# Optimization experiments

Hardware: AMD Instinct MI355X
Metric: run time of the kernel (lower is better)

The kernel has to match this reference:

```python
import jax, jax.numpy as jnp
import numpy as np

B_J0 = 0.01
BETA = 1.8
GAMMA = 0.5
LENS = 0.5
HIGHT = 0.15
SCALE = 6.0
H1, H2, D_IN, D_OUT = 256, 256, 700, 20
BATCH, T = 128, 250


def spike_fn(x):
    # forward of ActFun_adp: Heaviside
    return (x > 0).astype(x.dtype)


def mem_update_adp(inputs, mem, spike, tau_adp, b, tau_m):
    alpha = jnp.exp(-1.0 / tau_m)
    ro = jnp.exp(-1.0 / tau_adp)
    b = ro * b + (1.0 - ro) * spike
    B = B_J0 + BETA * b
    mem = mem * alpha + (1.0 - alpha) * inputs - B * spike
    spike = spike_fn(mem - B)
    return mem, spike, b


def setup_inputs() -> dict:
    key = jax.random.key(0)
    ks = jax.random.split(key, 16)
    inp = {
        "x": jax.random.uniform(ks[0], (BATCH, T, D_IN), jnp.float32),
        "mem1_0": jax.random.uniform(ks[1], (BATCH, H1), jnp.float32),
        "mem2_0": jax.random.uniform(ks[2], (BATCH, H2), jnp.float32),
        "memo_0": jax.random.uniform(ks[3], (BATCH, D_OUT), jnp.float32),
        "Wi1": jax.random.normal(ks[4], (H1, D_IN), jnp.float32) * 0.05,
        "bi1": jnp.zeros((H1,), jnp.float32),
        "W11": jax.random.normal(ks[5], (H1, H1), jnp.float32) * 0.05,
        "b11": jnp.zeros((H1,), jnp.float32),
        "W12": jax.random.normal(ks[6], (H2, H1), jnp.float32) * 0.05,
        "b12": jnp.zeros((H2,), jnp.float32),
        "W22": jax.random.normal(ks[7], (H2, H2), jnp.float32) * 0.05,
        "b22": jnp.zeros((H2,), jnp.float32),
        "Wo": jax.random.normal(ks[8], (D_OUT, H2), jnp.float32) * 0.05,
        "bo": jnp.zeros((D_OUT,), jnp.float32),
        "tau_adp_h1": 150.0 + 10.0 * jax.random.normal(ks[9], (H1,), jnp.float32),
        "tau_adp_h2": 150.0 + 10.0 * jax.random.normal(ks[10], (H2,), jnp.float32),
        "tau_m_h1": 20.0 + 5.0 * jax.random.normal(ks[11], (H1,), jnp.float32),
        "tau_m_h2": 20.0 + 5.0 * jax.random.normal(ks[12], (H2,), jnp.float32),
        "tau_m_o": 20.0 + 5.0 * jax.random.normal(ks[13], (D_OUT,), jnp.float32),
    }
    return inp


def reference(x, mem1_0, mem2_0, memo_0, Wi1, bi1, W11, b11, W12, b12,
              W22, b22, Wo, bo, tau_adp_h1, tau_adp_h2, tau_m_h1, tau_m_h2, tau_m_o):
    B = x.shape[0]
    sp1_0 = jnp.zeros_like(mem1_0)
    sp2_0 = jnp.zeros_like(mem2_0)
    b1_0 = jnp.full_like(mem1_0, B_J0)
    b2_0 = jnp.full_like(mem2_0, B_J0)
    acc0 = jnp.zeros((B, Wo.shape[0]), x.dtype)
    alpha_o = jnp.exp(-1.0 / tau_m_o)

    def step(carry, inp):
        x_t, i = inp
        mem1, sp1, b1, mem2, sp2, b2, memo, acc = carry
        h1_in = x_t @ Wi1.T + bi1 + sp1 @ W11.T + b11
        mem1, sp1, b1 = mem_update_adp(h1_in, mem1, sp1, tau_adp_h1, b1, tau_m_h1)
        h2_in = sp1 @ W12.T + b12 + sp2 @ W22.T + b22
        mem2, sp2, b2 = mem_update_adp(h2_in, mem2, sp2, tau_adp_h2, b2, tau_m_h2)
        memo = memo * alpha_o + (1.0 - alpha_o) * (sp2 @ Wo.T + bo)
        acc = acc + jnp.where(i > 10, jax.nn.softmax(memo, axis=1), 0.0)
        return (mem1, sp1, b1, mem2, sp2, b2, memo, acc), None

    xs = jnp.swapaxes(x, 0, 1)  # [T, B, D_in]
    ts = jnp.arange(xs.shape[0])
    carry, _ = jax.lax.scan(step, (mem1_0, sp1_0, b1_0, mem2_0, sp2_0, b2_0, memo_0, acc0), (xs, ts))
    return carry[-1]  # accumulated softmax output [B, D_out]
```

## Files before the change

### kernel.cpp

```cpp
#include <hip/hip_runtime.h>
#include <math.h>

#define BATCH 128
#define T 250
#define D_IN 700
#define H 256
#define D_OUT 20

typedef float v2f __attribute__((ext_vector_type(2)));
typedef __attribute__((ext_vector_type(8))) short bf16x8;
typedef __attribute__((ext_vector_type(4))) float f32x4;
typedef __attribute__((ext_vector_type(4))) unsigned u32x4;

static __device__ __forceinline__ unsigned short f2b(float f) {
    unsigned u = __float_as_uint(f);
    u += 0x7FFFu + ((u >> 16) & 1u);
    return (unsigned short)(u >> 16);
}

static __device__ __forceinline__ void bar() {
    asm volatile("s_waitcnt lgkmcnt(0)" ::: "memory");
    __builtin_amdgcn_s_barrier();
    asm volatile("" ::: "memory");
}

#define PIDX(c) (10 * ((c) >> 3) + ((c) & 7))

#define N_C  (257 * 512)
#define N_WP (256 * 704)

__global__ void prep_k(const float* __restrict__ Wi1, const float* __restrict__ W11,
                       const float* __restrict__ W12, const float* __restrict__ W22,
                       const float* __restrict__ Wo,
                       unsigned short* __restrict__ Wi1p, unsigned short* __restrict__ C1,
                       unsigned short* __restrict__ C2) {
    int idx = blockIdx.x * 256 + threadIdx.x;
    if (idx < N_C) {
        int k = idx >> 9, p = idx & 511;
        float v = 0.f;
        if (k < H) v = (p < 256) ? W12[p * H + k] : W11[(p - 256) * H + k];
        C1[idx] = f2b(v);
        return;
    }
    idx -= N_C;
    if (idx < N_C) {
        int k = idx >> 9, p = idx & 511;
        float v = 0.f;
        if (k < H) {
            if (p < 256) v = W22[p * H + k];
            else if (p - 256 < D_OUT) v = Wo[(p - 256) * H + k];
        }
        C2[idx] = f2b(v);
        return;
    }
    idx -= N_C;
    if (idx < N_WP) {
        int h = idx / 704, k = idx - h * 704;
        Wi1p[idx] = (k < D_IN) ? f2b(Wi1[h * D_IN + k]) : (unsigned short)0;
    }
}

__global__ __launch_bounds__(256) void gemm_u_k(const float* __restrict__ x,
                                                const unsigned short* __restrict__ Wi1p,
                                                const float* __restrict__ bi1,
                                                float* __restrict__ U) {
    const int lane = threadIdx.x & 63;
    const int wv = threadIdx.x >> 6;
    const int quad = lane >> 4;
    const int nl = lane & 15;
    const int mbase = blockIdx.x * 64 + wv * 16;
    const int m = mbase + nl;

    f32x4 acc[16];
#pragma unroll
    for (int i = 0; i < 16; ++i) acc[i] = (f32x4)(0.f);

    float bias[16];
#pragma unroll
    for (int nt = 0; nt < 16; ++nt) bias[nt] = bi1[nt * 16 + nl];

    const float* xrow = x + (size_t)m * D_IN;
    const unsigned short* brow = Wi1p + nl * 704 + quad * 8;

    for (int k0 = 0; k0 < 704; k0 += 32) {
        int ka = k0 + quad * 8;
        int ka2 = (ka + 4 <= 696) ? ka + 4 : 696;
        float4 q0 = *(const float4*)(xrow + ka);
        float4 q1 = *(const float4*)(xrow + ka2);
        bf16x8 af;
        af[0] = (short)f2b(q0.x); af[1] = (short)f2b(q0.y);
        af[2] = (short)f2b(q0.z); af[3] = (short)f2b(q0.w);
        af[4] = (short)f2b(q1.x); af[5] = (short)f2b(q1.y);
        af[6] = (short)f2b(q1.z); af[7] = (short)f2b(q1.w);

        const unsigned short* bp = brow + k0;
        bf16x8 bf[16];
#pragma unroll
        for (int nt = 0; nt < 16; ++nt)
            bf[nt] = *(const bf16x8*)(bp + nt * 16 * 704);
#pragma unroll
        for (int nt = 0; nt < 16; ++nt)
            acc[nt] = __builtin_amdgcn_mfma_f32_16x16x32_bf16(af, bf[nt], acc[nt], 0, 0, 0);
    }

#pragma unroll
    for (int nt = 0; nt < 16; ++nt) {
#pragma unroll
        for (int r = 0; r < 4; ++r) {
            U[(size_t)(mbase + quad * 4 + r) * H + nt * 16 + nl] = acc[nt][r] + bias[nt];
        }
    }
}

static __device__ __forceinline__ void ld8b(const unsigned* __restrict__ L, int c,
                                            const unsigned short* __restrict__ Cb,
                                            unsigned l8, u32x4* b) {
    uint4 ia = *(const uint4*)(L + c);
    uint4 ib = *(const uint4*)(L + c + 4);
    unsigned I[8] = {ia.x, ia.y, ia.z, ia.w, ib.x, ib.y, ib.z, ib.w};
#pragma unroll
    for (int jj = 0; jj < 8; ++jj)
        b[jj] = *(const u32x4*)(Cb + ((unsigned)I[jj] << 9) + l8);
}

static __device__ __forceinline__ void acc8b(const u32x4* b, v2f* a) {
#pragma unroll
    for (int jj = 0; jj < 8; ++jj) {
#pragma unroll
        for (int q = 0; q < 4; ++q) {
            unsigned u = b[jj][q];
            v2f t;
            t.x = __uint_as_float(u << 16);
            t.y = __uint_as_float(u & 0xffff0000u);
            a[q] += t;
        }
    }
}

static __device__ __forceinline__ void gatherB(const unsigned* __restrict__ L, int n,
                                               const unsigned short* __restrict__ Cb,
                                               unsigned l8, v2f* a) {
    a[0] = (v2f)(0.f); a[1] = (v2f)(0.f); a[2] = (v2f)(0.f); a[3] = (v2f)(0.f);
    int nr = (n + 7) & ~7;
    if (nr == 0) return;
    u32x4 x[8], y[8];
    ld8b(L, 0, Cb, l8, x);
    if (nr == 8) { acc8b(x, a); return; }
    ld8b(L, 8, Cb, l8, y);
    int c = 16;
    for (; c + 16 <= nr; c += 16) {
        acc8b(x, a); ld8b(L, c, Cb, l8, x);
        acc8b(y, a); ld8b(L, c + 8, Cb, l8, y);
    }
    if (nr - c == 8) {
        acc8b(x, a); ld8b(L, c, Cb, l8, x);
        acc8b(y, a); acc8b(x, a);
    } else {
        acc8b(x, a); acc8b(y, a);
    }
}

__global__ __launch_bounds__(512, 1) void recurrent_k(
    const float* __restrict__ U,
    const float* __restrict__ mem1_0, const float* __restrict__ mem2_0,
    const float* __restrict__ memo_0,
    const float* __restrict__ b11v, const float* __restrict__ b12v,
    const float* __restrict__ b22v, const float* __restrict__ bov,
    const float* __restrict__ tau_adp_h1, const float* __restrict__ tau_adp_h2,
    const float* __restrict__ tau_m_h1, const float* __restrict__ tau_m_h2,
    const float* __restrict__ tau_m_o,
    const unsigned short* __restrict__ C1b, const unsigned short* __restrict__ C2b,
    float* __restrict__ out)
{
    const int tid = threadIdx.x;
    const int lane = tid & 63;
    const int w = tid >> 6;
    const bool trackA = (w < 4);
    const int wt = w & 3;
    const int bi = blockIdx.x;
    const int j = wt * 64 + lane;
    const unsigned l8 = (unsigned)lane * 8;

    __shared__ float PA[4][2][640];
    __shared__ float PB[4][3][640];
    __shared__ __align__(16) unsigned lists[8][128];

    for (int i = tid; i < 4 * 2 * 640; i += 512) ((float*)PA)[i] = 0.f;
    for (int i = tid; i < 4 * 3 * 640; i += 512) ((float*)PB)[i] = 0.f;
    __syncthreads();

    float mem1 = 0.f, b1 = 0.01f, spk1 = 0.f;
    float al1 = 0.f, ro1 = 0.f, oma1 = 0.f, omr1 = 0.f, b11p = 0.f;
    if (trackA) {
        mem1 = mem1_0[bi * H + j];
        al1 = __expf(-1.f / tau_m_h1[j]);
        ro1 = __expf(-1.f / tau_adp_h1[j]);
        oma1 = 1.f - al1; omr1 = 1.f - ro1;
        b11p = b11v[j];
    }

    float mem2 = 0.f, b2 = 0.01f, spk2 = 0.f;
    float al2 = 0.f, ro2 = 0.f, oma2 = 0.f, omr2 = 0.f, bs2 = 0.f;
    if (!trackA) {
        mem2 = mem2_0[bi * H + j];
        al2 = __expf(-1.f / tau_m_h2[j]);
        ro2 = __expf(-1.f / tau_adp_h2[j]);
        oma2 = 1.f - al2; omr2 = 1.f - ro2;
        bs2 = b12v[j] + b22v[j];
    }

    float memo = 0.f, alo = 0.f, omo = 0.f, bop = 0.f, acco = 0.f;
    const bool outl = (w == 4 && lane < D_OUT);
    if (outl) {
        memo = memo_0[bi * D_OUT + lane];
        alo = __expf(-1.f / tau_m_o[lane]);
        omo = 1.f - alo;
        bop = bov[lane];
    }

    const float* Up = U + (size_t)bi * T * H + j;
    float u_cur = trackA ? *Up : 0.f;
    float u_nxt = 0.f;
    const unsigned long long below = (1ull << lane) - 1ull;

    const int pidx_self = 320 + PIDX(j);
    const int pidx_j = PIDX(j);
    const int pidx_out = 320 + PIDX(lane);

    for (int t = 0; t < 252; ++t) {
        const int rbA = (t + 1) & 1;
        const int wbA = t & 1;
        const int rsB = (t + 1) % 3;
        const int wsB = (t + 2) % 3;

        if (trackA && t < 250) {
            float g11 = PA[0][rbA][pidx_self] + PA[1][rbA][pidx_self] +
                        PA[2][rbA][pidx_self] + PA[3][rbA][pidx_self];
            float h1 = u_cur + b11p + g11;
            b1 = ro1 * b1 + omr1 * spk1;
            float B1 = 0.01f + 1.8f * b1;
            mem1 = mem1 * al1 + oma1 * h1 - B1 * spk1;
            spk1 = (mem1 - B1 > 0.f) ? 1.f : 0.f;

            unsigned long long m = __ballot(spk1 != 0.f);
            int n = __popcll(m);
            unsigned* L = lists[w];
            if (spk1 != 0.f) L[__popcll(m & below)] = (unsigned)j;
            L[n + lane] = 256u;
            asm volatile("s_waitcnt lgkmcnt(0)" ::: "memory");
            __builtin_amdgcn_wave_barrier();

            u_nxt = Up[H];
            Up += H;

            v2f a[4];
            gatherB(L, n, C1b, l8, a);

            float* pw = &PA[wt][wbA][10 * lane];
            *(v2f*)(pw + 0) = a[0];
            *(v2f*)(pw + 2) = a[1];
            *(v2f*)(pw + 4) = a[2];
            *(v2f*)(pw + 6) = a[3];
            u_cur = u_nxt;
        }

        if (w == 4 && t >= 2) {
            float e = 0.f;
            if (lane < D_OUT) {
                float aO = PB[0][rsB][pidx_out] + PB[1][rsB][pidx_out] +
                           PB[2][rsB][pidx_out] + PB[3][rsB][pidx_out];
                memo = memo * alo + omo * (bop + aO);
                e = __expf(memo);
            }
            if (t >= 13) {
                float s = e;
#pragma unroll
                for (int dd = 16; dd >= 1; dd >>= 1) s += __shfl_xor(s, dd, 32);
                if (lane < D_OUT) acco += __fdividef(e, s);
            }
        }

        if (!trackA && t >= 1 && t < 251) {
            float g12 = PA[0][rbA][pidx_j] + PA[1][rbA][pidx_j] +
                        PA[2][rbA][pidx_j] + PA[3][rbA][pidx_j];
            float g22 = PB[0][rsB][pidx_j] + PB[1][rsB][pidx_j] +
                        PB[2][rsB][pidx_j] + PB[3][rsB][pidx_j];
            float h2 = bs2 + g22 + g12;
            b2 = ro2 * b2 + omr2 * spk2;
            float B2 = 0.01f + 1.8f * b2;
            mem2 = mem2 * al2 + oma2 * h2 - B2 * spk2;
            spk2 = (mem2 - B2 > 0.f) ? 1.f : 0.f;

            unsigned long long m = __ballot(spk2 != 0.f);
            int n = __popcll(m);
            unsigned* L = lists[w];
            if (spk2 != 0.f) L[__popcll(m & below)] = (unsigned)j;
            L[n + lane] = 256u;
            asm volatile("s_waitcnt lgkmcnt(0)" ::: "memory");
            __builtin_amdgcn_wave_barrier();

            v2f a[4];
            gatherB(L, n, C2b, l8, a);

            float* pw = &PB[wt][wsB][10 * lane];
            *(v2f*)(pw + 0) = a[0];
            *(v2f*)(pw + 2) = a[1];
            *(v2f*)(pw + 4) = a[2];
            *(v2f*)(pw + 6) = a[3];
        }

        bar();
    }

    if (outl) out[bi * D_OUT + lane] = acco;
}

extern "C" void kernel_launch(void* const* d_in, const int* in_sizes, int n_in,
                              void* d_out, int out_size, void* d_ws, size_t ws_size,
                              hipStream_t stream) {
    const float* x          = (const float*)d_in[0];
    const float* mem1_0     = (const float*)d_in[1];
    const float* mem2_0     = (const float*)d_in[2];
    const float* memo_0     = (const float*)d_in[3];
    const float* Wi1        = (const float*)d_in[4];
    const float* bi1        = (const float*)d_in[5];
    const float* W11        = (const float*)d_in[6];
    const float* b11        = (const float*)d_in[7];
    const float* W12        = (const float*)d_in[8];
    const float* b12        = (const float*)d_in[9];
    const float* W22        = (const float*)d_in[10];
    const float* b22        = (const float*)d_in[11];
    const float* Wo         = (const float*)d_in[12];
    const float* bo         = (const float*)d_in[13];
    const float* tau_adp_h1 = (const float*)d_in[14];
    const float* tau_adp_h2 = (const float*)d_in[15];
    const float* tau_m_h1   = (const float*)d_in[16];
    const float* tau_m_h2   = (const float*)d_in[17];
    const float* tau_m_o    = (const float*)d_in[18];

    float* U = (float*)d_ws;
    unsigned short* C1b = (unsigned short*)(U + ((size_t)BATCH * T + 1) * H);
    unsigned short* C2b = C1b + N_C;
    unsigned short* Wi1p = C2b + N_C;

    int prep_total = 2 * N_C + N_WP;
    prep_k<<<(prep_total + 255) / 256, 256, 0, stream>>>(
        Wi1, W11, W12, W22, Wo, Wi1p, C1b, C2b);

    gemm_u_k<<<(BATCH * T) / 64, 256, 0, stream>>>(x, Wi1p, bi1, U);

    recurrent_k<<<BATCH, 512, 0, stream>>>(U, mem1_0, mem2_0, memo_0,
                                           b11, b12, b22, bo,
                                           tau_adp_h1, tau_adp_h2,
                                           tau_m_h1, tau_m_h2, tau_m_o,
                                           C1b, C2b, (float*)d_out);
}
```

Before: 384.9 us.

## Fuse input projection GEMM into recurrent kernel and shrink layer-2 gather payload

Removes the separate gemm_u_k launch and the U buffer in global memory. Instead, each recurrent block computes its own 16-timestep chunk of x·Wi1ᵀ with MFMA, interleaved across the idle parts of each step, and double-buffers the result in LDS. It also narrows the C2 table from 512 to 288 columns so the layer-2 gather loads only W22 plus the 20 output columns, shrinking the PB layout. The trade-off is extra per-step latency and more register and LDS pressure inside the serial recurrent loop, which runs only 128 blocks.

```diff
diff --git a/kernel.cpp b/kernel.cpp
--- a/kernel.cpp
+++ b/kernel.cpp
@@ -25,8 +25,10 @@
 }
 
 #define PIDX(c) (10 * ((c) >> 3) + ((c) & 7))
-
-#define N_C  (257 * 512)
+#define QIDX(c) (6 * ((c) >> 2) + ((c) & 3))
+
+#define N_C1 (257 * 512)
+#define N_C2 (257 * 288)
 #define N_WP (256 * 704)
 
 __global__ void prep_k(const float* __restrict__ Wi1, const float* __restrict__ W11,
@@ -35,16 +37,16 @@
                        unsigned short* __restrict__ Wi1p, unsigned short* __restrict__ C1,
                        unsigned short* __restrict__ C2) {
     int idx = blockIdx.x * 256 + threadIdx.x;
-    if (idx < N_C) {
+    if (idx < N_C1) {
         int k = idx >> 9, p = idx & 511;
         float v = 0.f;
         if (k < H) v = (p < 256) ? W12[p * H + k] : W11[(p - 256) * H + k];
         C1[idx] = f2b(v);
         return;
     }
-    idx -= N_C;
-    if (idx < N_C) {
-        int k = idx >> 9, p = idx & 511;
+    idx -= N_C1;
+    if (idx < N_C2) {
+        int k = idx / 288, p = idx - k * 288;
         float v = 0.f;
         if (k < H) {
             if (p < 256) v = W22[p * H + k];
@@ -53,62 +55,10 @@
         C2[idx] = f2b(v);
         return;
     }
-    idx -= N_C;
+    idx -= N_C2;
     if (idx < N_WP) {
         int h = idx / 704, k = idx - h * 704;
         Wi1p[idx] = (k < D_IN) ? f2b(Wi1[h * D_IN + k]) : (unsigned short)0;
-    }
-}
-
-__global__ __launch_bounds__(256) void gemm_u_k(const float* __restrict__ x,
-                                                const unsigned short* __restrict__ Wi1p,
-                                                const float* __restrict__ bi1,
-                                                float* __restrict__ U) {
-    const int lane = threadIdx.x & 63;
-    const int wv = threadIdx.x >> 6;
-    const int quad = lane >> 4;
-    const int nl = lane & 15;
-    const int mbase = blockIdx.x * 64 + wv * 16;
-    const int m = mbase + nl;
-
-    f32x4 acc[16];
-#pragma unroll
-    for (int i = 0; i < 16; ++i) acc[i] = (f32x4)(0.f);
-
-    float bias[16];
-#pragma unroll
-    for (int nt = 0; nt < 16; ++nt) bias[nt] = bi1[nt * 16 + nl];
-
-    const float* xrow = x + (size_t)m * D_IN;
-    const unsigned short* brow = Wi1p + nl * 704 + quad * 8;
-
-    for (int k0 = 0; k0 < 704; k0 += 32) {
-        int ka = k0 + quad * 8;
-        int ka2 = (ka + 4 <= 696) ? ka + 4 : 696;
-        float4 q0 = *(const float4*)(xrow + ka);
-        float4 q1 = *(const float4*)(xrow + ka2);
-        bf16x8 af;
-        af[0] = (short)f2b(q0.x); af[1] = (short)f2b(q0.y);
-        af[2] = (short)f2b(q0.z); af[3] = (short)f2b(q0.w);
-        af[4] = (short)f2b(q1.x); af[5] = (short)f2b(q1.y);
-        af[6] = (short)f2b(q1.z); af[7] = (short)f2b(q1.w);
-
-        const unsigned short* bp = brow + k0;
-        bf16x8 bf[16];
-#pragma unroll
-        for (int nt = 0; nt < 16; ++nt)
-            bf[nt] = *(const bf16x8*)(bp + nt * 16 * 704);
-#pragma unroll
-        for (int nt = 0; nt < 16; ++nt)
-            acc[nt] = __builtin_amdgcn_mfma_f32_16x16x32_bf16(af, bf[nt], acc[nt], 0, 0, 0);
-    }
-
-#pragma unroll
-    for (int nt = 0; nt < 16; ++nt) {
-#pragma unroll
-        for (int r = 0; r < 4; ++r) {
-            U[(size_t)(mbase + quad * 4 + r) * H + nt * 16 + nl] = acc[nt][r] + bias[nt];
-        }
     }
 }
 
@@ -160,8 +110,62 @@
     }
 }
 
+static __device__ __forceinline__ void ld8c(const unsigned* __restrict__ L, int c,
+                                            const unsigned short* __restrict__ Cb,
+                                            unsigned mo, unsigned ao,
+                                            uint2* m, unsigned* av) {
+    uint4 ia = *(const uint4*)(L + c);
+    uint4 ib = *(const uint4*)(L + c + 4);
+    unsigned I[8] = {ia.x, ia.y, ia.z, ia.w, ib.x, ib.y, ib.z, ib.w};
+#pragma unroll
+    for (int jj = 0; jj < 8; ++jj) {
+        const unsigned short* p = Cb + (unsigned)I[jj] * 288u;
+        m[jj] = *(const uint2*)(p + mo);
+        av[jj] = *(const unsigned*)(p + ao);
+    }
+}
+
+static __device__ __forceinline__ void acc8c(const uint2* m, const unsigned* av,
+                                             v2f* g, v2f& aA) {
+#pragma unroll
+    for (int jj = 0; jj < 8; ++jj) {
+        unsigned u0 = m[jj].x, u1 = m[jj].y, uA = av[jj];
+        v2f t0, t1, tA;
+        t0.x = __uint_as_float(u0 << 16); t0.y = __uint_as_float(u0 & 0xffff0000u);
+        t1.x = __uint_as_float(u1 << 16); t1.y = __uint_as_float(u1 & 0xffff0000u);
+        tA.x = __uint_as_float(uA << 16); tA.y = __uint_as_float(uA & 0xffff0000u);
+        g[0] += t0; g[1] += t1; aA += tA;
+    }
+}
+
+static __device__ __forceinline__ void gather2(const unsigned* __restrict__ L, int n,
+                                               const unsigned short* __restrict__ Cb,
+                                               unsigned mo, unsigned ao,
+                                               v2f* g, v2f& aA) {
+    g[0] = (v2f)(0.f); g[1] = (v2f)(0.f); aA = (v2f)(0.f);
+    int nr = (n + 7) & ~7;
+    if (nr == 0) return;
+    uint2 xm[8], ym[8]; unsigned xa[8], ya[8];
+    ld8c(L, 0, Cb, mo, ao, xm, xa);
+    if (nr == 8) { acc8c(xm, xa, g, aA); return; }
+    ld8c(L, 8, Cb, mo, ao, ym, ya);
+    int c = 16;
+    for (; c + 16 <= nr; c += 16) {
+        acc8c(xm, xa, g, aA); ld8c(L, c, Cb, mo, ao, xm, xa);
+        acc8c(ym, ya, g, aA); ld8c(L, c + 8, Cb, mo, ao, ym, ya);
+    }
+    if (nr - c == 8) {
+        acc8c(xm, xa, g, aA); ld8c(L, c, Cb, mo, ao, xm, xa);
+        acc8c(ym, ya, g, aA); acc8c(xm, xa, g, aA);
+    } else {
+        acc8c(xm, xa, g, aA); acc8c(ym, ya, g, aA);
+    }
+}
+
 __global__ __launch_bounds__(512, 1) void recurrent_k(
-    const float* __restrict__ U,
+    const float* __restrict__ x,
+    const unsigned short* __restrict__ Wi1p,
+    const float* __restrict__ bi1,
     const float* __restrict__ mem1_0, const float* __restrict__ mem2_0,
     const float* __restrict__ memo_0,
     const float* __restrict__ b11v, const float* __restrict__ b12v,
@@ -180,14 +184,18 @@
     const int bi = blockIdx.x;
     const int j = wt * 64 + lane;
     const unsigned l8 = (unsigned)lane * 8;
+    const unsigned mo = (unsigned)lane * 4;
+    const unsigned ao = 256u + 2u * (unsigned)(lane & 15);
+    const int quad = lane >> 4;
+    const int nl = lane & 15;
 
     __shared__ float PA[4][2][640];
-    __shared__ float PB[4][3][640];
+    __shared__ float PB[4][3][432];
+    __shared__ float Ubuf[2][16][260];
     __shared__ __align__(16) unsigned lists[8][128];
 
     for (int i = tid; i < 4 * 2 * 640; i += 512) ((float*)PA)[i] = 0.f;
-    for (int i = tid; i < 4 * 3 * 640; i += 512) ((float*)PB)[i] = 0.f;
-    __syncthreads();
+    for (int i = tid; i < 4 * 3 * 432; i += 512) ((float*)PB)[i] = 0.f;
 
     float mem1 = 0.f, b1 = 0.01f, spk1 = 0.f;
     float al1 = 0.f, ro1 = 0.f, oma1 = 0.f, omr1 = 0.f, b11p = 0.f;
@@ -218,14 +226,46 @@
         bop = bov[lane];
     }
 
-    const float* Up = U + (size_t)bi * T * H + j;
-    float u_cur = trackA ? *Up : 0.f;
-    float u_nxt = 0.f;
+    f32x4 uacc[2];
+    uacc[0] = (f32x4)(0.f); uacc[1] = (f32x4)(0.f);
+    float ubias[2];
+    ubias[0] = bi1[w * 32 + nl];
+    ubias[1] = bi1[w * 32 + 16 + nl];
+    const float* xb = x + (size_t)bi * T * D_IN;
+
+    {
+#pragma unroll 1
+        for (int kc = 0; kc < 22; ++kc) {
+            int ka = kc * 32 + quad * 8;
+            int ka2 = (ka + 4 <= 696) ? ka + 4 : 696;
+            const float* xrow = xb + (size_t)nl * D_IN;
+            float4 q0 = *(const float4*)(xrow + ka);
+            float4 q1 = *(const float4*)(xrow + ka2);
+            bf16x8 af;
+            af[0] = (short)f2b(q0.x); af[1] = (short)f2b(q0.y);
+            af[2] = (short)f2b(q0.z); af[3] = (short)f2b(q0.w);
+            af[4] = (short)f2b(q1.x); af[5] = (short)f2b(q1.y);
+            af[6] = (short)f2b(q1.z); af[7] = (short)f2b(q1.w);
+#pragma unroll
+            for (int tt = 0; tt < 2; ++tt) {
+                bf16x8 bfv = *(const bf16x8*)(Wi1p + (size_t)(w * 32 + tt * 16 + nl) * 704 + ka);
+                uacc[tt] = __builtin_amdgcn_mfma_f32_16x16x32_bf16(af, bfv, uacc[tt], 0, 0, 0);
+            }
+        }
+#pragma unroll
+        for (int tt = 0; tt < 2; ++tt)
+#pragma unroll
+            for (int r = 0; r < 4; ++r)
+                Ubuf[0][quad * 4 + r][w * 32 + tt * 16 + nl] = uacc[tt][r] + ubias[tt];
+        uacc[0] = (f32x4)(0.f); uacc[1] = (f32x4)(0.f);
+    }
+    __syncthreads();
+
     const unsigned long long below = (1ull << lane) - 1ull;
-
     const int pidx_self = 320 + PIDX(j);
     const int pidx_j = PIDX(j);
-    const int pidx_out = 320 + PIDX(lane);
+    const int qidx_j = QIDX(j);
+    const int qidx_out = 384 + 6 * (lane >> 2) + (lane & 3);
 
     for (int t = 0; t < 252; ++t) {
         const int rbA = (t + 1) & 1;
@@ -236,7 +276,8 @@
         if (trackA && t < 250) {
             float g11 = PA[0][rbA][pidx_self] + PA[1][rbA][pidx_self] +
                         PA[2][rbA][pidx_self] + PA[3][rbA][pidx_self];
-            float h1 = u_cur + b11p + g11;
+            float u = Ubuf[(t >> 4) & 1][t & 15][j];
+            float h1 = u + b11p + g11;
             b1 = ro1 * b1 + omr1 * spk1;
             float B1 = 0.01f + 1.8f * b1;
             mem1 = mem1 * al1 + oma1 * h1 - B1 * spk1;
@@ -250,9 +291,6 @@
             asm volatile("s_waitcnt lgkmcnt(0)" ::: "memory");
             __builtin_amdgcn_wave_barrier();
 
-            u_nxt = Up[H];
-            Up += H;
-
             v2f a[4];
             gatherB(L, n, C1b, l8, a);
 
@@ -261,14 +299,13 @@
             *(v2f*)(pw + 2) = a[1];
             *(v2f*)(pw + 4) = a[2];
             *(v2f*)(pw + 6) = a[3];
-            u_cur = u_nxt;
         }
 
         if (w == 4 && t >= 2) {
             float e = 0.f;
             if (lane < D_OUT) {
-                float aO = PB[0][rsB][pidx_out] + PB[1][rsB][pidx_out] +
-                           PB[2][rsB][pidx_out] + PB[3][rsB][pidx_out];
+                float aO = PB[0][rsB][qidx_out] + PB[1][rsB][qidx_out] +
+                           PB[2][rsB][qidx_out] + PB[3][rsB][qidx_out];
                 memo = memo * alo + omo * (bop + aO);
                 e = __expf(memo);
             }
@@ -283,8 +320,8 @@
         if (!trackA && t >= 1 && t < 251) {
             float g12 = PA[0][rbA][pidx_j] + PA[1][rbA][pidx_j] +
                         PA[2][rbA][pidx_j] + PA[3][rbA][pidx_j];
-            float g22 = PB[0][rsB][pidx_j] + PB[1][rsB][pidx_j] +
-                        PB[2][rsB][pidx_j] + PB[3][rsB][pidx_j];
+            float g22 = PB[0][rsB][qidx_j] + PB[1][rsB][qidx_j] +
+                        PB[2][rsB][qidx_j] + PB[3][rsB][qidx_j];
             float h2 = bs2 + g22 + g12;
             b2 = ro2 * b2 + omr2 * spk2;
             float B2 = 0.01f + 1.8f * b2;
@@ -299,14 +336,59 @@
             asm volatile("s_waitcnt lgkmcnt(0)" ::: "memory");
             __builtin_amdgcn_wave_barrier();
 
-            v2f a[4];
-            gatherB(L, n, C2b, l8, a);
-
-            float* pw = &PB[wt][wsB][10 * lane];
-            *(v2f*)(pw + 0) = a[0];
-            *(v2f*)(pw + 2) = a[1];
-            *(v2f*)(pw + 4) = a[2];
-            *(v2f*)(pw + 6) = a[3];
+            v2f g[2]; v2f aA;
+            gather2(L, n, C2b, mo, ao, g, aA);
+
+            float* pw = &PB[wt][wsB][6 * lane];
+            *(v2f*)(pw + 0) = g[0];
+            *(v2f*)(pw + 2) = g[1];
+            if (lane < 16) {
+                float* pa = &PB[wt][wsB][384 + 6 * (lane >> 1) + 2 * (lane & 1)];
+                *(v2f*)pa = aA;
+            }
+        }
+
+        {
+            int c = t >> 4;
+            int t0n = (c + 1) << 4;
+            if (t < 250 && t0n < 250) {
+                int wi = t & 15;
+                if (wi < 11) {
+#pragma unroll
+                    for (int kk = 0; kk < 2; ++kk) {
+                        int kc = 2 * wi + kk;
+                        int ka = kc * 32 + quad * 8;
+                        int ka2 = (ka + 4 <= 696) ? ka + 4 : 696;
+                        int row = t0n + nl;
+                        bf16x8 af;
+                        if (row < 250) {
+                            const float* xrow = xb + (size_t)row * D_IN;
+                            float4 q0 = *(const float4*)(xrow + ka);
+                            float4 q1 = *(const float4*)(xrow + ka2);
+                            af[0] = (short)f2b(q0.x); af[1] = (short)f2b(q0.y);
+                            af[2] = (short)f2b(q0.z); af[3] = (short)f2b(q0.w);
+                            af[4] = (short)f2b(q1.x); af[5] = (short)f2b(q1.y);
+                            af[6] = (short)f2b(q1.z); af[7] = (short)f2b(q1.w);
+                        } else {
+#pragma unroll
+                            for (int z = 0; z < 8; ++z) af[z] = 0;
+                        }
+#pragma unroll
+                        for (int tt = 0; tt < 2; ++tt) {
+                            bf16x8 bfv = *(const bf16x8*)(Wi1p + (size_t)(w * 32 + tt * 16 + nl) * 704 + ka);
+                            uacc[tt] = __builtin_amdgcn_mfma_f32_16x16x32_bf16(af, bfv, uacc[tt], 0, 0, 0);
+                        }
+                    }
+                } else if (wi == 11) {
+                    int nb = (c + 1) & 1;
+#pragma unroll
+                    for (int tt = 0; tt < 2; ++tt)
+#pragma unroll
+                        for (int r = 0; r < 4; ++r)
+                            Ubuf[nb][quad * 4 + r][w * 32 + tt * 16 + nl] = uacc[tt][r] + ubias[tt];
+                    uacc[0] = (f32x4)(0.f); uacc[1] = (f32x4)(0.f);
+                }
+            }
         }
 
         bar();
@@ -338,18 +420,16 @@
     const float* tau_m_h2   = (const float*)d_in[17];
     const float* tau_m_o    = (const float*)d_in[18];
 
-    float* U = (float*)d_ws;
-    unsigned short* C1b = (unsigned short*)(U + ((size_t)BATCH * T + 1) * H);
-    unsigned short* C2b = C1b + N_C;
-    unsigned short* Wi1p = C2b + N_C;
-
-    int prep_total = 2 * N_C + N_WP;
+    unsigned short* C1b  = (unsigned short*)d_ws;
+    unsigned short* C2b  = C1b + N_C1;
+    unsigned short* Wi1p = C2b + N_C2;
+
+    int prep_total = N_C1 + N_C2 + N_WP;
     prep_k<<<(prep_total + 255) / 256, 256, 0, stream>>>(
         Wi1, W11, W12, W22, Wo, Wi1p, C1b, C2b);
 
-    gemm_u_k<<<(BATCH * T) / 64, 256, 0, stream>>>(x, Wi1p, bi1, U);
-
-    recurrent_k<<<BATCH, 512, 0, stream>>>(U, mem1_0, mem2_0, memo_0,
+    recurrent_k<<<BATCH, 512, 0, stream>>>(x, Wi1p, bi1,
+                                           mem1_0, mem2_0, memo_0,
                                            b11, b12, b22, bo,
                                            tau_adp_h1, tau_adp_h2,
                                            tau_m_h1, tau_m_h2, tau_m_o,
```

Result: slower. 568.4 us (+47.7%).
